# Performance work log

Measured on AMD Instinct MI355X. Metric: run time of the kernel, lower is better.

## Reference

```python
import jax, jax.numpy as jnp
import numpy as np

B, N, C = 2, 384, 1024          # images, proposals/image, box_head feature dim
H_REPN = 256                    # RePN hidden
G_HID, HEADS = 256, 4           # GATConv hidden / heads
TOPK = 8
IMG_H, IMG_W = 800, 800
NEG_SLOPE = 0.2                 # PyG GATConv leaky_relu default


def _box_geom(bx):
    # normalized [x, y, w, h], matching _box_geom
    scale = jnp.array([IMG_W, IMG_H, IMG_W, IMG_H], dtype=bx.dtype)
    nb = bx / scale
    return jnp.stack([nb[:, 0], nb[:, 1], nb[:, 2] - nb[:, 0], nb[:, 3] - nb[:, 1]], axis=1)


def _gat_layer(x, src, tgt, W, att_src, att_dst, bias, heads, out_c):
    # PyG GATConv: messages flow src -> tgt, softmax over incoming edges at tgt
    n = x.shape[0]
    xw = (x @ W).reshape(n, heads, out_c)               # [N, H, F]
    a_s = jnp.sum(xw * att_src, axis=-1)                # [N, H]
    a_d = jnp.sum(xw * att_dst, axis=-1)                # [N, H]
    e = jax.nn.leaky_relu(a_s[src] + a_d[tgt], NEG_SLOPE)  # [E, H]
    e_max = jax.ops.segment_max(e, tgt, num_segments=n)    # stable softmax per target
    alpha = jnp.exp(e - e_max[tgt])
    denom = jax.ops.segment_sum(alpha, tgt, num_segments=n)
    alpha = alpha / jnp.maximum(denom, 1e-16)[tgt]          # [E, H]
    out = jax.ops.segment_sum(xw[src] * alpha[..., None], tgt, num_segments=n)
    return out.reshape(n, heads * out_c) + bias


def setup_inputs() -> dict:
    key = jax.random.key(0)
    ks = jax.random.split(key, 16)
    feats = jax.random.normal(ks[0], (B, N, C), dtype=jnp.float32)
    # boxes with x1<x2, y1<y2 inside the image
    xy = jax.random.uniform(ks[1], (B, N, 2), minval=0.0, maxval=650.0)
    wh = jax.random.uniform(ks[2], (B, N, 2), minval=10.0, maxval=150.0)
    boxes = jnp.concatenate([xy, xy + wh], axis=-1).astype(jnp.float32)
    s = 0.02
    params = {
        'fc1_w': jax.random.normal(ks[3], (2 * C + 4, H_REPN)) * s,
        'fc1_b': jnp.zeros((H_REPN,), jnp.float32),
        'fc2_w': jax.random.normal(ks[4], (H_REPN, 1)) * s,
        'fc2_b': jnp.zeros((1,), jnp.float32),
        'gat1_w': jax.random.normal(ks[5], (C + 4, HEADS * G_HID)) * s,
        'gat1_att_src': jax.random.normal(ks[6], (HEADS, G_HID)) * s,
        'gat1_att_dst': jax.random.normal(ks[7], (HEADS, G_HID)) * s,
        'gat1_b': jnp.zeros((HEADS * G_HID,), jnp.float32),
        'gat2_w': jax.random.normal(ks[8], (HEADS * G_HID, 2)) * s,
        'gat2_att_src': jax.random.normal(ks[9], (1, 2)) * s,
        'gat2_att_dst': jax.random.normal(ks[10], (1, 2)) * s,
        'gat2_b': jnp.zeros((2,), jnp.float32),
    }
    return {'feats': feats, 'boxes': boxes, **params}


def reference(feats, boxes, fc1_w, fc1_b, fc2_w, fc2_b,
              gat1_w, gat1_att_src, gat1_att_dst, gat1_b,
              gat2_w, gat2_att_src, gat2_att_dst, gat2_b):
    def single(f, bx):
        geom4 = _box_geom(bx)                               # [N, 4]
        x = jnp.concatenate([f, geom4], axis=1)             # [N, C+4]
        # RelationProposalNetwork: fc1(cat[f_i, f_j, |b_i-b_j|]) done as split matmuls
        Wa, Wb, Wg = fc1_w[:C], fc1_w[C:2 * C], fc1_w[2 * C:]
        p1 = f @ Wa                                         # [N, H]
        p2 = f @ Wb                                         # [N, H]
        gdiff = jnp.abs(bx[:, None, :] - bx[None, :, :])    # [N, N, 4]
        h = jax.nn.relu(p1[:, None, :] + p2[None, :, :] + gdiff @ Wg + fc1_b)
        rel = (h @ fc2_w)[..., 0] + fc2_b[0]                # [N, N]
        # _make_edge_index: mask diagonal, top-k per row; edge = [dst_node, neighbor]
        rn = rel - jnp.eye(N, dtype=rel.dtype) * 1e6
        nbr = jax.lax.top_k(rn, TOPK)[1]                    # [N, k]
        src = jnp.repeat(jnp.arange(N), TOPK)               # edge_index[0] (PyG source)
        tgt = nbr.reshape(-1)                               # edge_index[1] (PyG target)
        loop = jnp.arange(N)                                # GATConv add_self_loops=True
        src = jnp.concatenate([src, loop])
        tgt = jnp.concatenate([tgt, loop])
        h1 = jax.nn.relu(_gat_layer(x, src, tgt, gat1_w, gat1_att_src, gat1_att_dst, gat1_b, HEADS, G_HID))
        logits = _gat_layer(h1, src, tgt, gat2_w, gat2_att_src, gat2_att_dst, gat2_b, 1, 2)
        return logits                                       # [N, 2]
    return jax.vmap(single)(feats, boxes)
```

## Files before the change

### kernel.cpp

```cpp
#include <hip/hip_runtime.h>

#define BB 2
#define NN 384
#define CC 1024
#define HR 256
#define NHEADS 4
#define TOPK 8
#define CAP 448
#define NEG 0.2f

typedef __attribute__((ext_vector_type(8))) short bf16x8;
typedef __attribute__((ext_vector_type(4))) float f32x4;

__device__ __forceinline__ unsigned short f2bf(float v) {
    unsigned u = __float_as_uint(v);
    return (unsigned short)((u + 0x7FFFu + ((u >> 16) & 1u)) >> 16);
}
__device__ __forceinline__ float bf2f(unsigned short h) {
    return __uint_as_float((unsigned)h << 16);
}

__global__ __launch_bounds__(256) void k_prep(const float* __restrict__ feats,
        const float* __restrict__ boxes, const float* __restrict__ gat1_w,
        const float* __restrict__ fc1_w,
        uint4* __restrict__ Asw, uint4* __restrict__ Bsw,
        uint4* __restrict__ Ah, uint4* __restrict__ Al,
        uint4* __restrict__ Bh, uint4* __restrict__ Bl,
        float4* __restrict__ wgp, int* __restrict__ counts,
        float* __restrict__ xw2) {
    __shared__ float sw[32][65];
    int blk = blockIdx.x;
    int t = threadIdx.x;
    int gflat = blk * 256 + t;
    if (gflat < BB * NN) counts[gflat] = 0;
    if (gflat < BB * NN * 2) xw2[gflat] = 0.f;

    if (blk < 396) {
        int flat = gflat;
        int lane = flat & 63;
        int kc = (flat >> 6) % 33;
        int mt = flat / (33 * 64);
        int m = mt * 16 + (lane & 15);
        int k0 = kc * 32 + (lane >> 4) * 8;
        unsigned short vals[8];
        const float s = 1.0f / 800.0f;
#pragma unroll
        for (int j = 0; j < 8; j++) {
            int k = k0 + j;
            float v;
            if (k < CC) v = feats[(size_t)m * CC + k];
            else if (k < CC + 4) {
                const float* bx = boxes + (size_t)m * 4;
                int gk = k - CC;
                v = (gk == 0) ? bx[0] * s : (gk == 1) ? bx[1] * s
                  : (gk == 2) ? (bx[2] - bx[0]) * s : (bx[3] - bx[1]) * s;
            } else v = 0.f;
            vals[j] = f2bf(v);
        }
        uint4 pk;
        pk.x = (unsigned)vals[0] | ((unsigned)vals[1] << 16);
        pk.y = (unsigned)vals[2] | ((unsigned)vals[3] << 16);
        pk.z = (unsigned)vals[4] | ((unsigned)vals[5] << 16);
        pk.w = (unsigned)vals[6] | ((unsigned)vals[7] << 16);
        Asw[flat] = pk;
    } else if (blk < 924) {
        int blkrel = blk - 396;
        int ntg = blkrel / 33;
        int kc  = blkrel % 33;
        int k0 = kc * 32;
        int n0 = ntg * 64;
#pragma unroll
        for (int pass = 0; pass < 8; pass++) {
            int kl = pass * 4 + (t >> 6);
            int k = k0 + kl;
            int nl = t & 63;
            float v = (k < CC + 4) ? gat1_w[(size_t)k * 1024 + n0 + nl] : 0.f;
            sw[kl][nl] = v;
        }
        __syncthreads();
        int local_nt = t >> 6;
        int lane = t & 63;
        int nn = lane & 15;
        int q = lane >> 4;
        int nl = local_nt * 16 + nn;
        unsigned short vals[8];
#pragma unroll
        for (int j = 0; j < 8; j++) vals[j] = f2bf(sw[q * 8 + j][nl]);
        uint4 pk;
        pk.x = (unsigned)vals[0] | ((unsigned)vals[1] << 16);
        pk.y = (unsigned)vals[2] | ((unsigned)vals[3] << 16);
        pk.z = (unsigned)vals[4] | ((unsigned)vals[5] << 16);
        pk.w = (unsigned)vals[6] | ((unsigned)vals[7] << 16);
        int nt = ntg * 4 + local_nt;
        Bsw[(size_t)nt * 33 * 64 + kc * 64 + lane] = pk;
    } else if (blk < 1308) {
        int flat = gflat - 924 * 256;
        int lane = flat & 63;
        int kc = (flat >> 6) % 32;
        int mt = flat / (32 * 64);
        int m = mt * 16 + (lane & 15);
        int k0 = kc * 32 + (lane >> 4) * 8;
        unsigned short vh[8], vl[8];
        const float* src = feats + (size_t)m * CC + k0;
#pragma unroll
        for (int j = 0; j < 8; j++) {
            float v = src[j];
            unsigned short h = f2bf(v);
            vh[j] = h;
            vl[j] = f2bf(v - bf2f(h));
        }
        uint4 ph, pl;
        ph.x = (unsigned)vh[0] | ((unsigned)vh[1] << 16);
        ph.y = (unsigned)vh[2] | ((unsigned)vh[3] << 16);
        ph.z = (unsigned)vh[4] | ((unsigned)vh[5] << 16);
        ph.w = (unsigned)vh[6] | ((unsigned)vh[7] << 16);
        pl.x = (unsigned)vl[0] | ((unsigned)vl[1] << 16);
        pl.y = (unsigned)vl[2] | ((unsigned)vl[3] << 16);
        pl.z = (unsigned)vl[4] | ((unsigned)vl[5] << 16);
        pl.w = (unsigned)vl[6] | ((unsigned)vl[7] << 16);
        Ah[flat] = ph; Al[flat] = pl;
    } else if (blk < 1564) {
        int blkrel = blk - 1308;
        int ntg = blkrel / 32;
        int kc  = blkrel % 32;
        int k0 = kc * 32;
        int n0 = ntg * 64;
#pragma unroll
        for (int pass = 0; pass < 8; pass++) {
            int kl = pass * 4 + (t >> 6);
            int k = k0 + kl;
            int n = n0 + (t & 63);
            float v = (n < 256) ? fc1_w[(size_t)k * 256 + n]
                                : fc1_w[(size_t)(CC + k) * 256 + (n - 256)];
            sw[kl][t & 63] = v;
        }
        __syncthreads();
        int local_nt = t >> 6;
        int lane = t & 63;
        int nn = lane & 15;
        int q = lane >> 4;
        int nl = local_nt * 16 + nn;
        unsigned short vh[8], vl[8];
#pragma unroll
        for (int j = 0; j < 8; j++) {
            float v = sw[q * 8 + j][nl];
            unsigned short h = f2bf(v);
            vh[j] = h;
            vl[j] = f2bf(v - bf2f(h));
        }
        uint4 ph, pl;
        ph.x = (unsigned)vh[0] | ((unsigned)vh[1] << 16);
        ph.y = (unsigned)vh[2] | ((unsigned)vh[3] << 16);
        ph.z = (unsigned)vh[4] | ((unsigned)vh[5] << 16);
        ph.w = (unsigned)vh[6] | ((unsigned)vh[7] << 16);
        pl.x = (unsigned)vl[0] | ((unsigned)vl[1] << 16);
        pl.y = (unsigned)vl[2] | ((unsigned)vl[3] << 16);
        pl.z = (unsigned)vl[4] | ((unsigned)vl[5] << 16);
        pl.w = (unsigned)vl[6] | ((unsigned)vl[7] << 16);
        int nt = ntg * 4 + local_nt;
        size_t o = (size_t)nt * 32 * 64 + kc * 64 + lane;
        Bh[o] = ph; Bl[o] = pl;
    } else {
        int c = t;
        float4 w;
        w.x = fc1_w[(size_t)(2 * CC + 0) * HR + c];
        w.y = fc1_w[(size_t)(2 * CC + 1) * HR + c];
        w.z = fc1_w[(size_t)(2 * CC + 2) * HR + c];
        w.w = fc1_w[(size_t)(2 * CC + 3) * HR + c];
        wgp[c] = w;
    }
}

__global__ __launch_bounds__(512) void k_mm(const uint4* __restrict__ Ah,
        const uint4* __restrict__ Al, const uint4* __restrict__ Bh,
        const uint4* __restrict__ Bl, const float* __restrict__ fc1_b,
        float* __restrict__ p1, float* __restrict__ p2t,
        const uint4* __restrict__ Asw, const uint4* __restrict__ Bsw,
        float* __restrict__ xw1) {
    __shared__ float lds[4][64][8];
    int t = threadIdx.x;
    int w = t >> 6;
    int lane = t & 63;
    int g = w & 3;
    int kh = w >> 2;
    int blk0 = blockIdx.x;
    if (blk0 < 192) {
        int mtp = blk0 >> 3;
        int nt = (blk0 & 7) * 4 + g;
        int mt0 = mtp * 2;
        f32x4 acc0 = {0.f, 0.f, 0.f, 0.f};
        f32x4 acc1 = {0.f, 0.f, 0.f, 0.f};
        const uint4* pah0 = Ah + (size_t)mt0 * 32 * 64 + (size_t)kh * 16 * 64 + lane;
        const uint4* pal0 = Al + (size_t)mt0 * 32 * 64 + (size_t)kh * 16 * 64 + lane;
        const uint4* pbh = Bh + (size_t)nt * 32 * 64 + (size_t)kh * 16 * 64 + lane;
        const uint4* pbl = Bl + (size_t)nt * 32 * 64 + (size_t)kh * 16 * 64 + lane;
#pragma unroll 2
        for (int kc = 0; kc < 16; kc++) {
            uint4 ah0 = pah0[kc * 64];
            uint4 al0 = pal0[kc * 64];
            uint4 ah1 = pah0[kc * 64 + 2048];
            uint4 al1 = pal0[kc * 64 + 2048];
            uint4 bh = pbh[kc * 64];
            uint4 bl = pbl[kc * 64];
            acc0 = __builtin_amdgcn_mfma_f32_16x16x32_bf16(*(bf16x8*)&ah0, *(bf16x8*)&bh, acc0, 0, 0, 0);
            acc0 = __builtin_amdgcn_mfma_f32_16x16x32_bf16(*(bf16x8*)&ah0, *(bf16x8*)&bl, acc0, 0, 0, 0);
            acc0 = __builtin_amdgcn_mfma_f32_16x16x32_bf16(*(bf16x8*)&al0, *(bf16x8*)&bh, acc0, 0, 0, 0);
            acc1 = __builtin_amdgcn_mfma_f32_16x16x32_bf16(*(bf16x8*)&ah1, *(bf16x8*)&bh, acc1, 0, 0, 0);
            acc1 = __builtin_amdgcn_mfma_f32_16x16x32_bf16(*(bf16x8*)&ah1, *(bf16x8*)&bl, acc1, 0, 0, 0);
            acc1 = __builtin_amdgcn_mfma_f32_16x16x32_bf16(*(bf16x8*)&al1, *(bf16x8*)&bh, acc1, 0, 0, 0);
        }
        if (kh == 1) {
#pragma unroll
            for (int r = 0; r < 4; r++) { lds[g][lane][r] = acc0[r]; lds[g][lane][4 + r] = acc1[r]; }
        }
        __syncthreads();
        if (kh == 0) {
#pragma unroll
            for (int r = 0; r < 4; r++) { acc0[r] += lds[g][lane][r]; acc1[r] += lds[g][lane][4 + r]; }
            int col = nt * 16 + (lane & 15);
            int rbase = (lane >> 4) * 4;
            if (col < 256) {
                float bias = fc1_b[col];
#pragma unroll
                for (int r = 0; r < 4; r++) {
                    p1[(size_t)(mt0 * 16 + rbase + r) * 256 + col] = acc0[r] + bias;
                    p1[(size_t)(mt0 * 16 + 16 + rbase + r) * 256 + col] = acc1[r] + bias;
                }
            } else {
#pragma unroll
                for (int r = 0; r < 4; r++) {
                    int rr0 = mt0 * 16 + rbase + r;
                    int rr1 = rr0 + 16;
                    p2t[((size_t)(rr0 / NN) * 256 + (col - 256)) * NN + (rr0 % NN)] = acc0[r];
                    p2t[((size_t)(rr1 / NN) * 256 + (col - 256)) * NN + (rr1 % NN)] = acc1[r];
                }
            }
        }
    } else {
        int blk = blk0 - 192;
        int mtp = blk >> 4;
        int nt = (blk & 15) * 4 + g;
        int mt0 = mtp * 2;
        int nk = kh ? 16 : 17;
        f32x4 acc0 = {0.f, 0.f, 0.f, 0.f};
        f32x4 acc1 = {0.f, 0.f, 0.f, 0.f};
        const uint4* pa0 = Asw + (size_t)mt0 * 33 * 64 + (size_t)kh * 17 * 64 + lane;
        const uint4* pb = Bsw + (size_t)nt * 33 * 64 + (size_t)kh * 17 * 64 + lane;
#pragma unroll 4
        for (int kc = 0; kc < nk; kc++) {
            uint4 a0 = pa0[kc * 64];
            uint4 a1 = pa0[kc * 64 + 2112];
            uint4 bv = pb[kc * 64];
            acc0 = __builtin_amdgcn_mfma_f32_16x16x32_bf16(*(bf16x8*)&a0, *(bf16x8*)&bv, acc0, 0, 0, 0);
            acc1 = __builtin_amdgcn_mfma_f32_16x16x32_bf16(*(bf16x8*)&a1, *(bf16x8*)&bv, acc1, 0, 0, 0);
        }
        if (kh == 1) {
#pragma unroll
            for (int r = 0; r < 4; r++) { lds[g][lane][r] = acc0[r]; lds[g][lane][4 + r] = acc1[r]; }
        }
        __syncthreads();
        if (kh == 0) {
#pragma unroll
            for (int r = 0; r < 4; r++) { acc0[r] += lds[g][lane][r]; acc1[r] += lds[g][lane][4 + r]; }
            int col = nt * 16 + (lane & 15);
            int rbase = (lane >> 4) * 4;
#pragma unroll
            for (int r = 0; r < 4; r++) {
                xw1[(size_t)(mt0 * 16 + rbase + r) * 1024 + col] = acc0[r];
                xw1[(size_t)(mt0 * 16 + 16 + rbase + r) * 1024 + col] = acc1[r];
            }
        }
    }
}

__global__ __launch_bounds__(384) void k_relatt(const float* __restrict__ p1,
        const float* __restrict__ p2t, const float* __restrict__ boxes,
        const float4* __restrict__ wgp, const float* __restrict__ fc2_w,
        float* __restrict__ rel_a, float* __restrict__ rel_b,
        const float* __restrict__ xw1, const float* __restrict__ att_src,
        const float* __restrict__ att_dst, float* __restrict__ a_s,
        float* __restrict__ a_d) {
    int blk0 = blockIdx.x;
    if (blk0 < 768) {
        int blk = blk0;
        int p = blk >> 1;
        int ch = blk & 1;
        int b = p / (NN / 2);
        int i0 = (p - b * (NN / 2)) * 2;
        int row0 = b * NN + i0;
        int j = threadIdx.x;
        float a0 = boxes[(size_t)row0 * 4 + 0];
        float a1 = boxes[(size_t)row0 * 4 + 1];
        float a2 = boxes[(size_t)row0 * 4 + 2];
        float a3 = boxes[(size_t)row0 * 4 + 3];
        float c0 = boxes[(size_t)(row0 + 1) * 4 + 0];
        float c1 = boxes[(size_t)(row0 + 1) * 4 + 1];
        float c2 = boxes[(size_t)(row0 + 1) * 4 + 2];
        float c3 = boxes[(size_t)(row0 + 1) * 4 + 3];
        float4 bj = *(const float4*)(boxes + ((size_t)b * NN + j) * 4);
        float g00 = fabsf(a0 - bj.x), g01 = fabsf(a1 - bj.y);
        float g02 = fabsf(a2 - bj.z), g03 = fabsf(a3 - bj.w);
        float g10 = fabsf(c0 - bj.x), g11 = fabsf(c1 - bj.y);
        float g12 = fabsf(c2 - bj.z), g13 = fabsf(c3 - bj.w);
        const float* p1r0 = p1 + (size_t)row0 * HR + ch * 128;
        const float* p1r1 = p1r0 + HR;
        const float* p2b = p2t + (size_t)b * HR * NN + (size_t)ch * 128 * NN + j;
        const float4* wg = wgp + ch * 128;
        const float* w2 = fc2_w + ch * 128;
        float acc0 = 0.f, acc1 = 0.f;
#pragma unroll 8
        for (int c = 0; c < 128; c++) {
            float4 w = wg[c];
            float pa = p1r0[c];
            float pb = p1r1[c];
            float wc = w2[c];
            float p2v = p2b[(size_t)c * NN];
            float v0 = pa + p2v + g00 * w.x + g01 * w.y + g02 * w.z + g03 * w.w;
            float v1 = pb + p2v + g10 * w.x + g11 * w.y + g12 * w.z + g13 * w.w;
            acc0 += fmaxf(v0, 0.f) * wc;
            acc1 += fmaxf(v1, 0.f) * wc;
        }
        float* dst = ch ? rel_b : rel_a;
        dst[(size_t)row0 * NN + j] = acc0;
        dst[(size_t)(row0 + 1) * NN + j] = acc1;
    } else {
        int node = blk0 - 768;
        int t = threadIdx.x;
        if (t >= 256) return;
        int w = t >> 6;
        int lane = t & 63;
        const float4* xr = (const float4*)(xw1 + (size_t)node * 1024 + w * 256);
        const float4* sr = (const float4*)(att_src + w * 256);
        const float4* dr = (const float4*)(att_dst + w * 256);
        float4 x = xr[lane];
        float4 s = sr[lane];
        float4 d = dr[lane];
        float ps = x.x * s.x + x.y * s.y + x.z * s.z + x.w * s.w;
        float pd = x.x * d.x + x.y * d.y + x.z * d.z + x.w * d.w;
#pragma unroll
        for (int off = 32; off > 0; off >>= 1) {
            ps += __shfl_xor(ps, off);
            pd += __shfl_xor(pd, off);
        }
        if (lane == 0) {
            a_s[(size_t)node * NHEADS + w] = ps;
            a_d[(size_t)node * NHEADS + w] = pd;
        }
    }
}

__global__ __launch_bounds__(64) void k_topk_inv(const float* __restrict__ rel_a,
        const float* __restrict__ rel_b, int* __restrict__ counts,
        int* __restrict__ inlist) {
    int row = blockIdx.x;
    int b = row / NN;
    int i = row - b * NN;
    int t = threadIdx.x;
    const float* ra = rel_a + (size_t)row * NN;
    const float* rb = rel_b + (size_t)row * NN;
    float v[6]; int id[6];
#pragma unroll
    for (int q = 0; q < 6; q++) {
        int j = t + q * 64;
        float val = ra[j] + rb[j];
        if (j == i) val = -INFINITY;
        v[q] = val; id[q] = j;
    }
    int mine = -1;
    for (int k = 0; k < TOPK; k++) {
        float bv = -INFINITY; int bi = NN;
#pragma unroll
        for (int q = 0; q < 6; q++) {
            if (v[q] > bv || (v[q] == bv && id[q] < bi)) { bv = v[q]; bi = id[q]; }
        }
        for (int off = 32; off > 0; off >>= 1) {
            float ov = __shfl_down(bv, off);
            int   oi = __shfl_down(bi, off);
            if (ov > bv || (ov == bv && oi < bi)) { bv = ov; bi = oi; }
        }
        bi = __shfl(bi, 0);
        if (t == k) mine = bi;
#pragma unroll
        for (int q = 0; q < 6; q++) if (id[q] == bi) v[q] = -INFINITY;
    }
    if (t < TOPK) {
        int tg = b * NN + mine;
        int q = atomicAdd(&counts[tg], 1);
        inlist[(size_t)tg * CAP + q] = i;
    } else if (t == TOPK) {
        int q = atomicAdd(&counts[row], 1);
        inlist[(size_t)row * CAP + q] = i;
    }
}

__global__ __launch_bounds__(256) void k_agg1h(const int* __restrict__ counts,
        const int* __restrict__ inlist, const float* __restrict__ a_s,
        const float* __restrict__ a_d, const float* __restrict__ xw1,
        const float* __restrict__ gat1_b, const float* __restrict__ w2,
        float* __restrict__ xw2) {
    __shared__ int slist[CAP];
    __shared__ float walpha[CAP];
    __shared__ float redp[8];
    int blk = blockIdx.x;
    int node = blk >> 2;
    int h = blk & 3;
    int b = node / NN;
    int t = threadIdx.x;
    int wid = t >> 6;
    int lane = t & 63;
    int deg = counts[node];
    for (int e = t; e < deg; e += 256) slist[e] = inlist[(size_t)node * CAP + e];
    __syncthreads();
    if (t < 64) {
        float ad = a_d[(size_t)node * NHEADS + h];
        float vals[7];
        int cnt = 0;
        float vmax = -INFINITY;
        for (int e = t; e < deg; e += 64) {
            float x = a_s[(size_t)(b * NN + slist[e]) * NHEADS + h] + ad;
            x = x >= 0.f ? x : NEG * x;
            vals[cnt++] = x;
            vmax = fmaxf(vmax, x);
        }
#pragma unroll
        for (int off = 32; off > 0; off >>= 1)
            vmax = fmaxf(vmax, __shfl_xor(vmax, off));
        float sum = 0.f;
        for (int i = 0; i < cnt; i++) {
            vals[i] = expf(vals[i] - vmax);
            sum += vals[i];
        }
#pragma unroll
        for (int off = 32; off > 0; off >>= 1)
            sum += __shfl_xor(sum, off);
        float inv = 1.f / fmaxf(sum, 1e-16f);
        cnt = 0;
        for (int e = t; e < deg; e += 64) walpha[e] = vals[cnt++] * inv;
    }
    __syncthreads();
    float acc = 0.f;
    for (int e = 0; e < deg; e++)
        acc += walpha[e] * xw1[(size_t)(b * NN + slist[e]) * 1024 + h * 256 + t];
    float o = fmaxf(acc + gat1_b[h * 256 + t], 0.f);
    int d = h * 256 + t;
    float p0 = o * w2[d * 2];
    float p1v = o * w2[d * 2 + 1];
#pragma unroll
    for (int off = 32; off > 0; off >>= 1) {
        p0 += __shfl_xor(p0, off);
        p1v += __shfl_xor(p1v, off);
    }
    if (lane == 0) { redp[wid] = p0; redp[4 + wid] = p1v; }
    __syncthreads();
    if (t == 0) {
        atomicAdd(&xw2[(size_t)node * 2],     redp[0] + redp[1] + redp[2] + redp[3]);
        atomicAdd(&xw2[(size_t)node * 2 + 1], redp[4] + redp[5] + redp[6] + redp[7]);
    }
}

__global__ __launch_bounds__(64) void k_agg2(const int* __restrict__ counts,
        const int* __restrict__ inlist, const float* __restrict__ xw2,
        const float* __restrict__ as2, const float* __restrict__ ad2,
        const float* __restrict__ b2, float* __restrict__ out) {
    int node = blockIdx.x;
    int b = node / NN;
    int lane = threadIdx.x;
    int deg = counts[node];
    float s0 = as2[0], s1 = as2[1];
    float d0 = ad2[0], d1 = ad2[1];
    float2 xwn = *(const float2*)(xw2 + (size_t)node * 2);
    float ad = xwn.x * d0 + xwn.y * d1;
    float vals[7], xs0[7], xs1[7];
    int cnt = 0;
    float vmax = -INFINITY;
    for (int e = lane; e < deg; e += 64) {
        int s = b * NN + inlist[(size_t)node * CAP + e];
        float2 xws = *(const float2*)(xw2 + (size_t)s * 2);
        float x = xws.x * s0 + xws.y * s1 + ad;
        x = x >= 0.f ? x : NEG * x;
        xs0[cnt] = xws.x; xs1[cnt] = xws.y; vals[cnt] = x; cnt++;
        vmax = fmaxf(vmax, x);
    }
#pragma unroll
    for (int off = 32; off > 0; off >>= 1)
        vmax = fmaxf(vmax, __shfl_xor(vmax, off));
    float sum = 0.f;
    for (int i = 0; i < cnt; i++) {
        vals[i] = expf(vals[i] - vmax);
        sum += vals[i];
    }
#pragma unroll
    for (int off = 32; off > 0; off >>= 1)
        sum += __shfl_xor(sum, off);
    float inv = 1.f / fmaxf(sum, 1e-16f);
    float a0 = 0.f, a1 = 0.f;
    for (int i = 0; i < cnt; i++) {
        a0 += vals[i] * xs0[i];
        a1 += vals[i] * xs1[i];
    }
#pragma unroll
    for (int off = 32; off > 0; off >>= 1) {
        a0 += __shfl_xor(a0, off);
        a1 += __shfl_xor(a1, off);
    }
    if (lane == 0) {
        out[(size_t)node * 2]     = a0 * inv + b2[0];
        out[(size_t)node * 2 + 1] = a1 * inv + b2[1];
    }
}

extern "C" void kernel_launch(void* const* d_in, const int* in_sizes, int n_in,
                              void* d_out, int out_size, void* d_ws, size_t ws_size,
                              hipStream_t stream) {
    const float* feats  = (const float*)d_in[0];
    const float* boxes  = (const float*)d_in[1];
    const float* fc1_w  = (const float*)d_in[2];
    const float* fc1_b  = (const float*)d_in[3];
    const float* fc2_w  = (const float*)d_in[4];
    const float* fc2_b  = (const float*)d_in[5];
    const float* gat1_w = (const float*)d_in[6];
    const float* g1as   = (const float*)d_in[7];
    const float* g1ad   = (const float*)d_in[8];
    const float* gat1_b = (const float*)d_in[9];
    const float* gat2_w = (const float*)d_in[10];
    const float* g2as   = (const float*)d_in[11];
    const float* g2ad   = (const float*)d_in[12];
    const float* gat2_b = (const float*)d_in[13];
    float* out = (float*)d_out;
    (void)fc2_b;

    char* ws = (char*)d_ws;
    size_t off = 0;
    auto alloc = [&](size_t bytes) -> void* {
        void* p = ws + off;
        off += (bytes + 255) / 256 * 256;
        return p;
    };
    int*   counts = (int*)alloc((size_t)BB * NN * 4);
    int*   inlist = (int*)alloc((size_t)BB * NN * CAP * 4);
    float* p1     = (float*)alloc((size_t)BB * NN * HR * 4);
    float* p2t    = (float*)alloc((size_t)BB * HR * NN * 4);
    float* rel_a  = (float*)alloc((size_t)BB * NN * NN * 4);
    float* rel_b  = (float*)alloc((size_t)BB * NN * NN * 4);
    float* xw1    = (float*)alloc((size_t)BB * NN * 1024 * 4);
    float* a_s1   = (float*)alloc((size_t)BB * NN * NHEADS * 4);
    float* a_d1   = (float*)alloc((size_t)BB * NN * NHEADS * 4);
    float* xw2    = (float*)alloc((size_t)BB * NN * 2 * 4);
    uint4* Asw    = (uint4*)alloc((size_t)48 * 33 * 64 * 16);
    uint4* Bsw    = (uint4*)alloc((size_t)64 * 33 * 64 * 16);
    uint4* Ah     = (uint4*)alloc((size_t)48 * 32 * 64 * 16);
    uint4* Al     = (uint4*)alloc((size_t)48 * 32 * 64 * 16);
    uint4* Bh     = (uint4*)alloc((size_t)32 * 32 * 64 * 16);
    uint4* Bl     = (uint4*)alloc((size_t)32 * 32 * 64 * 16);
    float4* wgp   = (float4*)alloc((size_t)HR * 16);
    (void)ws_size; (void)in_sizes; (void)n_in; (void)out_size;

    k_prep<<<1565, 256, 0, stream>>>(feats, boxes, gat1_w, fc1_w,
                                     Asw, Bsw, Ah, Al, Bh, Bl, wgp, counts, xw2);
    k_mm<<<576, 512, 0, stream>>>(Ah, Al, Bh, Bl, fc1_b, p1, p2t, Asw, Bsw, xw1);
    k_relatt<<<1536, 384, 0, stream>>>(p1, p2t, boxes, wgp, fc2_w, rel_a, rel_b,
                                       xw1, g1as, g1ad, a_s1, a_d1);
    k_topk_inv<<<BB * NN, 64, 0, stream>>>(rel_a, rel_b, counts, inlist);
    k_agg1h<<<BB * NN * NHEADS, 256, 0, stream>>>(counts, inlist, a_s1, a_d1, xw1,
                                                  gat1_b, gat2_w, xw2);
    k_agg2<<<BB * NN, 64, 0, stream>>>(counts, inlist, xw2, g2as, g2ad, gat2_b, out);
}
```

Before: 160.9 us.

## Fuse top-k edge selection into relation kernel and reuse bf16 feature tiles

```diff
diff --git a/kernel.cpp b/kernel.cpp
--- a/kernel.cpp
+++ b/kernel.cpp
@@ -24,7 +24,7 @@
         const float* __restrict__ boxes, const float* __restrict__ gat1_w,
         const float* __restrict__ fc1_w,
         uint4* __restrict__ Asw, uint4* __restrict__ Bsw,
-        uint4* __restrict__ Ah, uint4* __restrict__ Al,
+        uint4* __restrict__ Al,
         uint4* __restrict__ Bh, uint4* __restrict__ Bl,
         float4* __restrict__ wgp, int* __restrict__ counts,
         float* __restrict__ xw2) {
@@ -100,25 +100,20 @@
         int mt = flat / (32 * 64);
         int m = mt * 16 + (lane & 15);
         int k0 = kc * 32 + (lane >> 4) * 8;
-        unsigned short vh[8], vl[8];
+        unsigned short vl[8];
         const float* src = feats + (size_t)m * CC + k0;
 #pragma unroll
         for (int j = 0; j < 8; j++) {
             float v = src[j];
             unsigned short h = f2bf(v);
-            vh[j] = h;
             vl[j] = f2bf(v - bf2f(h));
         }
-        uint4 ph, pl;
-        ph.x = (unsigned)vh[0] | ((unsigned)vh[1] << 16);
-        ph.y = (unsigned)vh[2] | ((unsigned)vh[3] << 16);
-        ph.z = (unsigned)vh[4] | ((unsigned)vh[5] << 16);
-        ph.w = (unsigned)vh[6] | ((unsigned)vh[7] << 16);
+        uint4 pl;
         pl.x = (unsigned)vl[0] | ((unsigned)vl[1] << 16);
         pl.y = (unsigned)vl[2] | ((unsigned)vl[3] << 16);
         pl.z = (unsigned)vl[4] | ((unsigned)vl[5] << 16);
         pl.w = (unsigned)vl[6] | ((unsigned)vl[7] << 16);
-        Ah[flat] = ph; Al[flat] = pl;
+        Al[flat] = pl;
     } else if (blk < 1564) {
         int blkrel = blk - 1308;
         int ntg = blkrel / 32;
@@ -171,12 +166,11 @@
     }
 }
 
-__global__ __launch_bounds__(512) void k_mm(const uint4* __restrict__ Ah,
+__global__ __launch_bounds__(512) void k_mm(const uint4* __restrict__ Asw,
         const uint4* __restrict__ Al, const uint4* __restrict__ Bh,
         const uint4* __restrict__ Bl, const float* __restrict__ fc1_b,
         float* __restrict__ p1, float* __restrict__ p2t,
-        const uint4* __restrict__ Asw, const uint4* __restrict__ Bsw,
-        float* __restrict__ xw1) {
+        const uint4* __restrict__ Bsw, float* __restrict__ xw1) {
     __shared__ float lds[4][64][8];
     int t = threadIdx.x;
     int w = t >> 6;
@@ -190,7 +184,7 @@
         int mt0 = mtp * 2;
         f32x4 acc0 = {0.f, 0.f, 0.f, 0.f};
         f32x4 acc1 = {0.f, 0.f, 0.f, 0.f};
-        const uint4* pah0 = Ah + (size_t)mt0 * 32 * 64 + (size_t)kh * 16 * 64 + lane;
+        const uint4* pah0 = Asw + (size_t)mt0 * 33 * 64 + (size_t)kh * 16 * 64 + lane;
         const uint4* pal0 = Al + (size_t)mt0 * 32 * 64 + (size_t)kh * 16 * 64 + lane;
         const uint4* pbh = Bh + (size_t)nt * 32 * 64 + (size_t)kh * 16 * 64 + lane;
         const uint4* pbl = Bl + (size_t)nt * 32 * 64 + (size_t)kh * 16 * 64 + lane;
@@ -198,7 +192,7 @@
         for (int kc = 0; kc < 16; kc++) {
             uint4 ah0 = pah0[kc * 64];
             uint4 al0 = pal0[kc * 64];
-            uint4 ah1 = pah0[kc * 64 + 2048];
+            uint4 ah1 = pah0[kc * 64 + 2112];
             uint4 al1 = pal0[kc * 64 + 2048];
             uint4 bh = pbh[kc * 64];
             uint4 bl = pbl[kc * 64];
@@ -276,19 +270,20 @@
 __global__ __launch_bounds__(384) void k_relatt(const float* __restrict__ p1,
         const float* __restrict__ p2t, const float* __restrict__ boxes,
         const float4* __restrict__ wgp, const float* __restrict__ fc2_w,
-        float* __restrict__ rel_a, float* __restrict__ rel_b,
+        int* __restrict__ counts, int* __restrict__ inlist,
         const float* __restrict__ xw1, const float* __restrict__ att_src,
         const float* __restrict__ att_dst, float* __restrict__ a_s,
         float* __restrict__ a_d) {
+    __shared__ float cv[2][48];
+    __shared__ int   ci[2][48];
     int blk0 = blockIdx.x;
-    if (blk0 < 768) {
-        int blk = blk0;
-        int p = blk >> 1;
-        int ch = blk & 1;
-        int b = p / (NN / 2);
-        int i0 = (p - b * (NN / 2)) * 2;
+    if (blk0 < 384) {
+        int b = blk0 / 192;
+        int i0 = (blk0 - b * 192) * 2;
         int row0 = b * NN + i0;
         int j = threadIdx.x;
+        int wid = j >> 6;
+        int lane = j & 63;
         float a0 = boxes[(size_t)row0 * 4 + 0];
         float a1 = boxes[(size_t)row0 * 4 + 1];
         float a2 = boxes[(size_t)row0 * 4 + 2];
@@ -302,29 +297,70 @@
         float g02 = fabsf(a2 - bj.z), g03 = fabsf(a3 - bj.w);
         float g10 = fabsf(c0 - bj.x), g11 = fabsf(c1 - bj.y);
         float g12 = fabsf(c2 - bj.z), g13 = fabsf(c3 - bj.w);
-        const float* p1r0 = p1 + (size_t)row0 * HR + ch * 128;
+        const float* p1r0 = p1 + (size_t)row0 * HR;
         const float* p1r1 = p1r0 + HR;
-        const float* p2b = p2t + (size_t)b * HR * NN + (size_t)ch * 128 * NN + j;
-        const float4* wg = wgp + ch * 128;
-        const float* w2 = fc2_w + ch * 128;
+        const float* p2b = p2t + (size_t)b * HR * NN + j;
         float acc0 = 0.f, acc1 = 0.f;
 #pragma unroll 8
-        for (int c = 0; c < 128; c++) {
-            float4 w = wg[c];
+        for (int c = 0; c < HR; c++) {
+            float4 w = wgp[c];
             float pa = p1r0[c];
             float pb = p1r1[c];
-            float wc = w2[c];
+            float wc = fc2_w[c];
             float p2v = p2b[(size_t)c * NN];
             float v0 = pa + p2v + g00 * w.x + g01 * w.y + g02 * w.z + g03 * w.w;
             float v1 = pb + p2v + g10 * w.x + g11 * w.y + g12 * w.z + g13 * w.w;
             acc0 += fmaxf(v0, 0.f) * wc;
             acc1 += fmaxf(v1, 0.f) * wc;
         }
-        float* dst = ch ? rel_b : rel_a;
-        dst[(size_t)row0 * NN + j] = acc0;
-        dst[(size_t)(row0 + 1) * NN + j] = acc1;
+        if (j == i0) acc0 = -INFINITY;
+        if (j == i0 + 1) acc1 = -INFINITY;
+#pragma unroll
+        for (int r = 0; r < 2; r++) {
+            float val = r ? acc1 : acc0;
+            int idx = j;
+            for (int k = 0; k < TOPK; k++) {
+                float bv = val; int bi = idx;
+#pragma unroll
+                for (int off = 32; off > 0; off >>= 1) {
+                    float ov = __shfl_xor(bv, off);
+                    int   oi = __shfl_xor(bi, off);
+                    if (ov > bv || (ov == bv && oi < bi)) { bv = ov; bi = oi; }
+                }
+                if (lane == k) { cv[r][wid * 8 + k] = bv; ci[r][wid * 8 + k] = bi; }
+                if (idx == bi) val = -INFINITY;
+            }
+        }
+        __syncthreads();
+        if (wid < 2) {
+            int r = wid;
+            float val = (lane < 48) ? cv[r][lane] : -INFINITY;
+            int idx = (lane < 48) ? ci[r][lane] : NN;
+            int mine = -1;
+            for (int k = 0; k < TOPK; k++) {
+                float bv = val; int bi = idx;
+#pragma unroll
+                for (int off = 32; off > 0; off >>= 1) {
+                    float ov = __shfl_xor(bv, off);
+                    int   oi = __shfl_xor(bi, off);
+                    if (ov > bv || (ov == bv && oi < bi)) { bv = ov; bi = oi; }
+                }
+                if (lane == k) mine = bi;
+                if (idx == bi) val = -INFINITY;
+            }
+            int i = i0 + r;
+            int rowg = b * NN + i;
+            if (lane < TOPK) {
+                int tg = b * NN + mine;
+                int q = atomicAdd(&counts[tg], 1);
+                inlist[(size_t)tg * CAP + q] = i;
+            } else if (lane == TOPK) {
+                int q = atomicAdd(&counts[rowg], 1);
+                inlist[(size_t)rowg * CAP + q] = i;
+            }
+        }
     } else {
-        int node = blk0 - 768;
+        int node = blk0 - 384;
         int t = threadIdx.x;
         if (t >= 256) return;
         int w = t >> 6;
@@ -346,50 +382,6 @@
             a_s[(size_t)node * NHEADS + w] = ps;
             a_d[(size_t)node * NHEADS + w] = pd;
         }
-    }
-}
-
-__global__ __launch_bounds__(64) void k_topk_inv(const float* __restrict__ rel_a,
-        const float* __restrict__ rel_b, int* __restrict__ counts,
-        int* __restrict__ inlist) {
-    int row = blockIdx.x;
-    int b = row / NN;
-    int i = row - b * NN;
-    int t = threadIdx.x;
-    const float* ra = rel_a + (size_t)row * NN;
-    const float* rb = rel_b + (size_t)row * NN;
-    float v[6]; int id[6];
-#pragma unroll
-    for (int q = 0; q < 6; q++) {
-        int j = t + q * 64;
-        float val = ra[j] + rb[j];
-        if (j == i) val = -INFINITY;
-        v[q] = val; id[q] = j;
-    }
-    int mine = -1;
-    for (int k = 0; k < TOPK; k++) {
-        float bv = -INFINITY; int bi = NN;
-#pragma unroll
-        for (int q = 0; q < 6; q++) {
-            if (v[q] > bv || (v[q] == bv && id[q] < bi)) { bv = v[q]; bi = id[q]; }
-        }
-        for (int off = 32; off > 0; off >>= 1) {
-            float ov = __shfl_down(bv, off);
-            int   oi = __shfl_down(bi, off);
-            if (ov > bv || (ov == bv && oi < bi)) { bv = ov; bi = oi; }
-        }
-        bi = __shfl(bi, 0);
-        if (t == k) mine = bi;
-#pragma unroll
-        for (int q = 0; q < 6; q++) if (id[q] == bi) v[q] = -INFINITY;
-    }
-    if (t < TOPK) {
-        int tg = b * NN + mine;
-        int q = atomicAdd(&counts[tg], 1);
-        inlist[(size_t)tg * CAP + q] = i;
-    } else if (t == TOPK) {
-        int q = atomicAdd(&counts[row], 1);
-        inlist[(size_t)row * CAP + q] = i;
     }
 }
 
@@ -540,15 +532,12 @@
     int*   inlist = (int*)alloc((size_t)BB * NN * CAP * 4);
     float* p1     = (float*)alloc((size_t)BB * NN * HR * 4);
     float* p2t    = (float*)alloc((size_t)BB * HR * NN * 4);
-    float* rel_a  = (float*)alloc((size_t)BB * NN * NN * 4);
-    float* rel_b  = (float*)alloc((size_t)BB * NN * NN * 4);
     float* xw1    = (float*)alloc((size_t)BB * NN * 1024 * 4);
     float* a_s1   = (float*)alloc((size_t)BB * NN * NHEADS * 4);
     float* a_d1   = (float*)alloc((size_t)BB * NN * NHEADS * 4);
     float* xw2    = (float*)alloc((size_t)BB * NN * 2 * 4);
     uint4* Asw    = (uint4*)alloc((size_t)48 * 33 * 64 * 16);
     uint4* Bsw    = (uint4*)alloc((size_t)64 * 33 * 64 * 16);
-    uint4* Ah     = (uint4*)alloc((size_t)48 * 32 * 64 * 16);
     uint4* Al     = (uint4*)alloc((size_t)48 * 32 * 64 * 16);
     uint4* Bh     = (uint4*)alloc((size_t)32 * 32 * 64 * 16);
     uint4* Bl     = (uint4*)alloc((size_t)32 * 32 * 64 * 16);
@@ -556,11 +545,10 @@
     (void)ws_size; (void)in_sizes; (void)n_in; (void)out_size;
 
     k_prep<<<1565, 256, 0, stream>>>(feats, boxes, gat1_w, fc1_w,
-                                     Asw, Bsw, Ah, Al, Bh, Bl, wgp, counts, xw2);
-    k_mm<<<576, 512, 0, stream>>>(Ah, Al, Bh, Bl, fc1_b, p1, p2t, Asw, Bsw, xw1);
-    k_relatt<<<1536, 384, 0, stream>>>(p1, p2t, boxes, wgp, fc2_w, rel_a, rel_b,
+                                     Asw, Bsw, Al, Bh, Bl, wgp, counts, xw2);
+    k_mm<<<576, 512, 0, stream>>>(Asw, Al, Bh, Bl, fc1_b, p1, p2t, Bsw, xw1);
+    k_relatt<<<1152, 384, 0, stream>>>(p1, p2t, boxes, wgp, fc2_w, counts, inlist,
                                        xw1, g1as, g1ad, a_s1, a_d1);
-    k_topk_inv<<<BB * NN, 64, 0, stream>>>(rel_a, rel_b, counts, inlist);
     k_agg1h<<<BB * NN * NHEADS, 256, 0, stream>>>(counts, inlist, a_s1, a_d1, xw1,
                                                   gat1_b, gat2_w, xw2);
     k_agg2<<<BB * NN, 64, 0, stream>>>(counts, inlist, xw2, g2as, g2ad, gat2_b, out);
```

New measurement: 174.4 us. 8.4% more time.
